# Performance work log

Hardware: AMD Instinct MI355X
Metric: run time of the kernel (lower is better)

The kernel has to match this reference:

```python
import jax, jax.numpy as jnp
import numpy as np

N_NODES = 10000
N_EDGES = 160000
B = 128
HEADS = 4
DIMS = [36, 128, 256, 512]
NEG_SLOPE = 0.2  # PyG GATConv default


def setup_inputs() -> dict:
    key = jax.random.key(0)
    ks = jax.random.split(key, 32)
    inp = {}
    inp["x"] = jax.random.normal(ks[0], (N_NODES, DIMS[0]), jnp.float32)
    inp["edge_index"] = jax.random.randint(ks[1], (2, N_EDGES), 0, N_NODES)
    inp["batch"] = jnp.sort(jax.random.randint(ks[2], (N_NODES,), 0, B))
    ki = 3
    for i in range(3):
        din, dout = DIMS[i], DIMS[i + 1]
        C = dout // HEADS
        inp[f"gcn_w{i}"] = jax.random.normal(ks[ki], (din, dout), jnp.float32) * (din ** -0.5); ki += 1
        inp[f"gcn_b{i}"] = jnp.zeros((dout,), jnp.float32)
        inp[f"gat_w{i}"] = jax.random.normal(ks[ki], (dout, dout), jnp.float32) * (dout ** -0.5); ki += 1
        inp[f"gat_as{i}"] = jax.random.normal(ks[ki], (HEADS, C), jnp.float32) * 0.1; ki += 1
        inp[f"gat_ad{i}"] = jax.random.normal(ks[ki], (HEADS, C), jnp.float32) * 0.1; ki += 1
        inp[f"gat_b{i}"] = jnp.zeros((dout,), jnp.float32)
    D = DIMS[-1]
    inp["ap_w1"] = jax.random.normal(ks[ki], (D, D // 2), jnp.float32) * (D ** -0.5); ki += 1
    inp["ap_b1"] = jnp.zeros((D // 2,), jnp.float32)
    inp["ap_w2"] = jax.random.normal(ks[ki], (D // 2, 1), jnp.float32) * ((D // 2) ** -0.5); ki += 1
    inp["ap_b2"] = jnp.zeros((1,), jnp.float32)
    return inp


def _gcn(x, w, b, src, dst, n):
    # PyG GCNConv: add self-loops, symmetric deg^-1/2 normalization, bias after agg
    h = x @ w  # [N, dout]
    deg = jax.ops.segment_sum(jnp.ones_like(dst, dtype=h.dtype), dst, n) + 1.0  # incl. self-loop
    dinv = deg ** -0.5
    norm = dinv[src] * dinv[dst]  # [E]
    agg = jax.ops.segment_sum(h[src] * norm[:, None], dst, n)
    agg = agg + h * (dinv * dinv)[:, None]  # self-loop messages
    return agg + b


def _gat(x, w, a_s, a_d, b, src, dst, n):
    # PyG GATConv: self-loops, leaky-relu logits, segment softmax over dst, concat heads
    C = w.shape[1] // HEADS
    h = (x @ w).reshape(n, HEADS, C)
    alpha_src = (h * a_s).sum(-1)  # [N, H]
    alpha_dst = (h * a_d).sum(-1)  # [N, H]
    loop = jnp.arange(n)
    s = jnp.concatenate([src, loop])
    d = jnp.concatenate([dst, loop])
    e = jax.nn.leaky_relu(alpha_src[s] + alpha_dst[d], NEG_SLOPE)  # [E+N, H]
    m = jax.ops.segment_max(e, d, n)
    ex = jnp.exp(e - m[d])
    den = jax.ops.segment_sum(ex, d, n)
    alpha = ex / den[d]  # [E+N, H]
    out = jax.ops.segment_sum(h[s] * alpha[:, :, None], d, n)  # [N, H, C]
    return out.reshape(n, HEADS * C) + b


def _forward(x, edge_index, batch, params, ap_w1, ap_b1, ap_w2, ap_b2):
    src, dst = edge_index[0], edge_index[1]
    n = x.shape[0]
    x_in = x
    n_layers = len(params)
    for i, (gw, gb, aw, a_s, a_d, ab) in enumerate(params):
        h = jax.nn.relu(_gcn(x, gw, gb, src, dst, n))  # dropout is identity in eval
        x = h + _gat(h, aw, a_s, a_d, ab, src, dst, n)
        if i < n_layers - 1:
            if x.shape[-1] == x_in.shape[-1]:
                x = x + x_in
            x_in = x
    # attention pooling (global softmax then per-graph masked renorm)
    a = jnp.tanh(x @ ap_w1 + ap_b1) @ ap_w2 + ap_b2  # [N, 1]
    a = jax.nn.softmax(a, axis=0)
    mask = jax.nn.one_hot(batch, B, dtype=x.dtype)  # [N, B]
    aw_ = a * mask
    aw_ = aw_ / (aw_.sum(0, keepdims=True) + 1e-8)
    graph_emb = aw_.T @ x  # [B, D]
    cnt = jax.ops.segment_sum(jnp.ones((n,), x.dtype), batch, B)
    ssum = jax.ops.segment_sum(x, batch, B)
    mean = ssum / jnp.maximum(cnt, 1.0)[:, None]
    smax = jax.ops.segment_max(x, batch, B)
    return jnp.concatenate([graph_emb, mean, smax, ssum], axis=1)  # [B, 4*D]


def reference(x, edge_index, batch,
              gcn_w0, gcn_b0, gat_w0, gat_as0, gat_ad0, gat_b0,
              gcn_w1, gcn_b1, gat_w1, gat_as1, gat_ad1, gat_b1,
              gcn_w2, gcn_b2, gat_w2, gat_as2, gat_ad2, gat_b2,
              ap_w1, ap_b1, ap_w2, ap_b2):
    params = [
        (gcn_w0, gcn_b0, gat_w0, gat_as0, gat_ad0, gat_b0),
        (gcn_w1, gcn_b1, gat_w1, gat_as1, gat_ad1, gat_b1),
        (gcn_w2, gcn_b2, gat_w2, gat_as2, gat_ad2, gat_b2),
    ]
    return _forward(x, edge_index, batch, params, ap_w1, ap_b1, ap_w2, ap_b2)
```

## Files before the change

### kernel.cpp

```cpp
#include <hip/hip_runtime.h>
#include <math.h>

#define NN 10000
#define NE 160000
#define NB 128
#define NH 4
#define DOUT 512
#define NEG 0.2f

typedef __attribute__((ext_vector_type(8))) short short8;
typedef __attribute__((ext_vector_type(4))) float f32x4;
typedef __attribute__((ext_vector_type(4))) unsigned short us4;

__device__ __forceinline__ float leakyf(float v){ return v > 0.f ? v : NEG*v; }
__device__ __forceinline__ void fma4(float4& a, const float4 v, float w){
  a.x += v.x*w; a.y += v.y*w; a.z += v.z*w; a.w += v.w*w;
}
__device__ __forceinline__ unsigned short f2bf(float f){
  unsigned int u = __float_as_uint(f);
  u += 0x7FFFu + ((u >> 16) & 1u);
  return (unsigned short)(u >> 16);
}
__device__ __forceinline__ float bf2f(unsigned short h){
  return __uint_as_float(((unsigned int)h) << 16);
}
__device__ __forceinline__ void split2(float v, unsigned short& h, unsigned short& l){
  h = f2bf(v);
  l = f2bf(v - bf2f(h));
}
__device__ __forceinline__ void store_hl(unsigned short* H, unsigned short* L,
                                         size_t base, float4 v){
  us4 h, l; unsigned short hh, ll;
  split2(v.x, hh, ll); h[0]=hh; l[0]=ll;
  split2(v.y, hh, ll); h[1]=hh; l[1]=ll;
  split2(v.z, hh, ll); h[2]=hh; l[2]=ll;
  split2(v.w, hh, ll); h[3]=hh; l[3]=ll;
  *(us4*)&H[base] = h;
  *(us4*)&L[base] = l;
}
__device__ __forceinline__ float4 load_hl(const unsigned short* __restrict__ H,
                                          const unsigned short* __restrict__ L, size_t base){
  us4 h = *(const us4*)&H[base];
  us4 l = *(const us4*)&L[base];
  return make_float4(bf2f(h[0])+bf2f(l[0]), bf2f(h[1])+bf2f(l[1]),
                     bf2f(h[2])+bf2f(l[2]), bf2f(h[3])+bf2f(l[3]));
}
__device__ __forceinline__ void gl_lds16(const unsigned short* g, unsigned short* l){
  __builtin_amdgcn_global_load_lds(
      (const __attribute__((address_space(1))) unsigned int*)g,
      (__attribute__((address_space(3))) unsigned int*)l, 16, 0, 0);
}

__global__ void k_count(const int* __restrict__ dst, int* __restrict__ cnt){
  int e = blockIdx.x*blockDim.x + threadIdx.x;
  if (e < NE) atomicAdd(&cnt[dst[e]], 1);
}
__global__ void k_scan(const int* __restrict__ cnt, int* __restrict__ rowptr,
                       float* __restrict__ dinv, int* __restrict__ cursor,
                       const int* __restrict__ batch, int* __restrict__ starts){
  __shared__ int part[256];
  const int CH = (NN + 255) / 256;
  int t = threadIdx.x;
  int base = t * CH;
  int s = 0;
  for (int i = 0; i < CH; i++){ int idx = base + i; if (idx < NN) s += cnt[idx]; }
  part[t] = s; __syncthreads();
  for (int o = 1; o < 256; o <<= 1){
    int v = 0;
    if (t >= o) v = part[t - o];
    __syncthreads();
    if (t >= o) part[t] += v;
    __syncthreads();
  }
  int pre = (t == 0) ? 0 : part[t - 1];
  for (int i = 0; i < CH; i++){
    int idx = base + i;
    if (idx < NN){
      int c = cnt[idx];
      rowptr[idx] = pre; pre += c;
      dinv[idx] = rsqrtf((float)c + 1.f);
      cursor[idx] = 0;
    }
  }
  if (t == 255) rowptr[NN] = part[255];
  if (t <= NB){
    int lo = 0, hi = NN;
    while (lo < hi){ int mid = (lo + hi) >> 1; if (batch[mid] < t) lo = mid + 1; else hi = mid; }
    starts[t] = lo;
  }
}
__global__ void k_fill(const int* __restrict__ src, const int* __restrict__ dst,
                       const int* __restrict__ rowptr, int* __restrict__ cursor,
                       int* __restrict__ colidx){
  int e = blockIdx.x*blockDim.x + threadIdx.x;
  if (e >= NE) return;
  int d = dst[e];
  int pos = atomicAdd(&cursor[d], 1);
  colidx[rowptr[d] + pos] = src[e];
}

struct AllConv {
  const float* src[8];
  unsigned short* dh[8];
  unsigned short* dl[8];
  int K[8], Mm[8], Kp[8], tot[8];
};
__global__ void k_convall(AllConv a){
  int j = blockIdx.y;
  int idx = blockIdx.x*blockDim.x + threadIdx.x;
  if (idx >= a.tot[j]) return;
  float v;
  if (j == 0){
    int n = idx >> 6, c = idx & 63;
    v = (c < 36) ? a.src[0][n*36 + c] : 0.f;
  } else {
    int Kp = a.Kp[j], K = a.K[j], M = a.Mm[j];
    int kk = idx % Kp, m = idx / Kp;
    v = (kk < K) ? a.src[j][(size_t)kk*M + m] : 0.f;
  }
  unsigned short h, l; split2(v, h, l);
  a.dh[j][idx] = h; a.dl[j][idx] = l;
}

#define GBM 64
#define GBN 128
#define GBK 32
__global__ __launch_bounds__(256) void k_gemm_bf3(
    const unsigned short* __restrict__ Ah, const unsigned short* __restrict__ Al,
    const unsigned short* __restrict__ Bh, const unsigned short* __restrict__ Bl,
    float* __restrict__ C, int N, int Kp, int M, int mode,
    const float* __restrict__ bias, unsigned short* __restrict__ outH,
    unsigned short* __restrict__ outL,
    const float* __restrict__ a_s, const float* __restrict__ a_d,
    float* __restrict__ as_o, float* __restrict__ ad_o, int Cdim){
  __shared__ unsigned short AsH[GBM*GBK], AsL[GBM*GBK];
  __shared__ unsigned short BsH[GBN*GBK], BsL[GBN*GBK];
  __shared__ float sred[2][GBM][4];
  int gx = M / GBN;
  int gy = (N + GBM - 1) / GBM;
  const int G = 8;
  int bid = blockIdx.x;
  int full = gy / G;
  int bid_full = full * G * gx;
  int by, bx;
  if (bid < bid_full){
    int g = bid / (G*gx); int rem = bid % (G*gx);
    by = g*G + rem % G; bx = rem / G;
  } else {
    int rem = bid - bid_full; int rows = gy - full*G;
    by = full*G + rem % rows; bx = rem / rows;
  }
  int row0 = by * GBM, col0 = bx * GBN;
  int t = threadIdx.x;
  int w = t >> 6, L = t & 63;
  int lm = L & 15, lq = L >> 4;
  int wc = w * 32;

  int sr = L >> 2, sc = L & 3;
  int art = w*16 + sr;
  int ga  = (sc - ((art >> 1) & 3)) & 3;
  int agrow = min(row0 + art, N-1);
  int brt0 = w*16 + sr;
  int brt1 = (w+4)*16 + sr;
  int gb0 = (sc - ((brt0 >> 1) & 3)) & 3;
  int gb1 = (sc - ((brt1 >> 1) & 3)) & 3;
  int bgrow0 = col0 + brt0, bgrow1 = col0 + brt1;

  int rc = (lq + (lm >> 1)) & 3;
  int aoff[4], boff[2];
#pragma unroll
  for (int mi = 0; mi < 4; mi++) aoff[mi] = (mi*16 + lm)*32 + rc*8;
#pragma unroll
  for (int ni = 0; ni < 2; ni++) boff[ni] = (wc + ni*16 + lm)*32 + rc*8;

  f32x4 acc[4][2];
#pragma unroll
  for (int i = 0; i < 4; i++)
#pragma unroll
    for (int j = 0; j < 2; j++) acc[i][j] = (f32x4){0.f,0.f,0.f,0.f};

  int nk = Kp / GBK;
  for (int kt = 0; kt < nk; kt++){
    int k0 = kt * GBK;
    if (kt) __syncthreads();
    gl_lds16(&Ah[(size_t)agrow*Kp + k0 + ga*8],  &AsH[w*512]);
    gl_lds16(&Al[(size_t)agrow*Kp + k0 + ga*8],  &AsL[w*512]);
    gl_lds16(&Bh[(size_t)bgrow0*Kp + k0 + gb0*8], &BsH[w*512]);
    gl_lds16(&Bh[(size_t)bgrow1*Kp + k0 + gb1*8], &BsH[(w+4)*512]);
    gl_lds16(&Bl[(size_t)bgrow0*Kp + k0 + gb0*8], &BsL[w*512]);
    gl_lds16(&Bl[(size_t)bgrow1*Kp + k0 + gb1*8], &BsL[(w+4)*512]);
    __syncthreads();

    short8 ah[4], al[4], bh[2], bl[2];
#pragma unroll
    for (int mi = 0; mi < 4; mi++){
      ah[mi] = *(const short8*)&AsH[aoff[mi]];
      al[mi] = *(const short8*)&AsL[aoff[mi]];
    }
#pragma unroll
    for (int ni = 0; ni < 2; ni++){
      bh[ni] = *(const short8*)&BsH[boff[ni]];
      bl[ni] = *(const short8*)&BsL[boff[ni]];
    }
#pragma unroll
    for (int mi = 0; mi < 4; mi++)
#pragma unroll
      for (int ni = 0; ni < 2; ni++){
        acc[mi][ni] = __builtin_amdgcn_mfma_f32_16x16x32_bf16(ah[mi], bh[ni], acc[mi][ni], 0, 0, 0);
        acc[mi][ni] = __builtin_amdgcn_mfma_f32_16x16x32_bf16(ah[mi], bl[ni], acc[mi][ni], 0, 0, 0);
        acc[mi][ni] = __builtin_amdgcn_mfma_f32_16x16x32_bf16(al[mi], bh[ni], acc[mi][ni], 0, 0, 0);
      }
  }
  if (mode == 1){
#pragma unroll
    for (int mi = 0; mi < 4; mi++)
#pragma unroll
      for (int ni = 0; ni < 2; ni++){
#pragma unroll
        for (int r = 0; r < 4; r++){
          int row = row0 + mi*16 + lq*4 + r;
          int col = col0 + wc + ni*16 + lm;
          if (row < N){
            float v = fmaxf(acc[mi][ni][r] + bias[col], 0.f);
            unsigned short hh, ll; split2(v, hh, ll);
            outH[(size_t)row*M + col] = hh;
            outL[(size_t)row*M + col] = ll;
          }
        }
      }
  } else {
#pragma unroll
    for (int mi = 0; mi < 4; mi++)
#pragma unroll
      for (int ni = 0; ni < 2; ni++){
#pragma unroll
        for (int r = 0; r < 4; r++){
          int row = row0 + mi*16 + lq*4 + r;
          int col = col0 + wc + ni*16 + lm;
          if (row < N) C[(size_t)row*M + col] = acc[mi][ni][r];
        }
      }
  }
  if (mode == 2){
    float sA0 = a_s[col0 + wc + lm], sA1 = a_s[col0 + wc + 16 + lm];
    float dA0 = a_d[col0 + wc + lm], dA1 = a_d[col0 + wc + 16 + lm];
#pragma unroll
    for (int mi = 0; mi < 4; mi++)
#pragma unroll
      for (int r = 0; r < 4; r++){
        float vs = acc[mi][0][r]*sA0 + acc[mi][1][r]*sA1;
        float vd = acc[mi][0][r]*dA0 + acc[mi][1][r]*dA1;
#pragma unroll
        for (int o = 1; o <= 8; o <<= 1){
          vs += __shfl_xor(vs, o);
          vd += __shfl_xor(vd, o);
        }
        if (lm == 0){
          int row = mi*16 + lq*4 + r;
          sred[0][row][w] = vs;
          sred[1][row][w] = vd;
        }
      }
    __syncthreads();
    if (t < GBM){
      int n = row0 + t;
      if (n < N){
        int wph = Cdim >> 5;
        int nheads = 4 / wph;
        for (int g = 0; g < nheads; g++){
          float ss = 0.f, dd = 0.f;
          for (int q = 0; q < wph; q++){
            ss += sred[0][t][g*wph + q];
            dd += sred[1][t][g*wph + q];
          }
          int hd = (col0 + g*wph*32) / Cdim;
          as_o[n*NH + hd] = ss;
          ad_o[n*NH + hd] = dd;
        }
      }
    }
  }
}

__global__ __launch_bounds__(256) void k_gcn_pre(
    const unsigned short* __restrict__ inH, const unsigned short* __restrict__ inL,
    const float* __restrict__ dinv,
    const int* __restrict__ rowptr, const int* __restrict__ colidx,
    unsigned short* __restrict__ outH, unsigned short* __restrict__ outL,
    int Kp, int nchunk){
  int bid = blockIdx.x;
  int chunk = bid % nchunk, grp = bid / nchunk;
  int t = threadIdx.x;
  int sub = t & 15;
  int n = grp*16 + (t >> 4);
  if (n >= NN) return;
  int f0 = chunk*64 + sub*4;
  int b = rowptr[n], e = rowptr[n+1];
  float dn = dinv[n];
  float4 a0 = make_float4(0,0,0,0), a1 = make_float4(0,0,0,0);
  float4 a2 = make_float4(0,0,0,0), a3 = make_float4(0,0,0,0);
  int j = b;
  for (; j + 3 < e; j += 4){
    int s0 = colidx[j], s1 = colidx[j+1], s2 = colidx[j+2], s3 = colidx[j+3];
    float w0 = dinv[s0], w1 = dinv[s1], w2 = dinv[s2], w3 = dinv[s3];
    float4 v0 = load_hl(inH, inL, (size_t)s0*Kp + f0);
    float4 v1 = load_hl(inH, inL, (size_t)s1*Kp + f0);
    float4 v2 = load_hl(inH, inL, (size_t)s2*Kp + f0);
    float4 v3 = load_hl(inH, inL, (size_t)s3*Kp + f0);
    fma4(a0, v0, w0*dn); fma4(a1, v1, w1*dn);
    fma4(a2, v2, w2*dn); fma4(a3, v3, w3*dn);
  }
  for (; j < e; j++){
    int s = colidx[j];
    float4 v = load_hl(inH, inL, (size_t)s*Kp + f0);
    fma4(a0, v, dinv[s]*dn);
  }
  float4 acc = make_float4(a0.x+a1.x+a2.x+a3.x, a0.y+a1.y+a2.y+a3.y,
                           a0.z+a1.z+a2.z+a3.z, a0.w+a1.w+a2.w+a3.w);
  float4 sv = load_hl(inH, inL, (size_t)n*Kp + f0);
  float dn2 = dn*dn;
  acc.x += sv.x*dn2; acc.y += sv.y*dn2; acc.z += sv.z*dn2; acc.w += sv.w*dn2;
  store_hl(outH, outL, (size_t)n*Kp + f0, acc);
}

__global__ void k_gat_maxden(const int* __restrict__ rowptr, const int* __restrict__ colidx,
                             const float* __restrict__ as_, const float* __restrict__ ad_,
                             float* __restrict__ eself, float* __restrict__ den,
                             float* __restrict__ ealpha){
  int idx = blockIdx.x*blockDim.x + threadIdx.x;
  if (idx >= NN*NH) return;
  int n = idx >> 2, hd = idx & 3;
  float adn = ad_[idx];
  float selflog = leakyf(as_[idx] + adn);
  int b = rowptr[n], e = rowptr[n+1];
  float m0 = selflog, m1 = -INFINITY, m2 = -INFINITY, m3 = -INFINITY;
  int j = b;
  for (; j + 3 < e; j += 4){
    int s0 = colidx[j], s1 = colidx[j+1], s2 = colidx[j+2], s3 = colidx[j+3];
    float l0 = leakyf(as_[s0*NH + hd] + adn), l1 = leakyf(as_[s1*NH + hd] + adn);
    float l2 = leakyf(as_[s2*NH + hd] + adn), l3 = leakyf(as_[s3*NH + hd] + adn);
    ealpha[(size_t)(j+0)*NH + hd] = l0; ealpha[(size_t)(j+1)*NH + hd] = l1;
    ealpha[(size_t)(j+2)*NH + hd] = l2; ealpha[(size_t)(j+3)*NH + hd] = l3;
    m0 = fmaxf(m0, l0); m1 = fmaxf(m1, l1);
    m2 = fmaxf(m2, l2); m3 = fmaxf(m3, l3);
  }
  for (; j < e; j++){
    float l = leakyf(as_[colidx[j]*NH + hd] + adn);
    ealpha[(size_t)j*NH + hd] = l;
    m0 = fmaxf(m0, l);
  }
  float m = fmaxf(fmaxf(m0, m1), fmaxf(m2, m3));
  float es = expf(selflog - m);
  float d0 = es, d1 = 0.f, d2 = 0.f, d3 = 0.f;
  j = b;
  for (; j + 3 < e; j += 4){
    float v0 = expf(ealpha[(size_t)(j+0)*NH + hd] - m);
    float v1 = expf(ealpha[(size_t)(j+1)*NH + hd] - m);
    float v2 = expf(ealpha[(size_t)(j+2)*NH + hd] - m);
    float v3 = expf(ealpha[(size_t)(j+3)*NH + hd] - m);
    ealpha[(size_t)(j+0)*NH + hd] = v0; ealpha[(size_t)(j+1)*NH + hd] = v1;
    ealpha[(size_t)(j+2)*NH + hd] = v2; ealpha[(size_t)(j+3)*NH + hd] = v3;
    d0 += v0; d1 += v1; d2 += v2; d3 += v3;
  }
  for (; j < e; j++){
    float v = expf(ealpha[(size_t)j*NH + hd] - m);
    ealpha[(size_t)j*NH + hd] = v;
    d0 += v;
  }
  eself[idx] = es;
  den[idx] = (d0 + d1) + (d2 + d3);
}
__global__ __launch_bounds__(256) void k_gat_gather(
    const float* __restrict__ hg,
    const unsigned short* __restrict__ inH, const unsigned short* __restrict__ inL,
    const int* __restrict__ rowptr, const int* __restrict__ colidx,
    const float* __restrict__ ealpha, const float* __restrict__ eself,
    const float* __restrict__ den, const float* __restrict__ ab,
    unsigned short* __restrict__ outH, unsigned short* __restrict__ outL,
    int M, int C, int nchunk){
  int bid = blockIdx.x;
  int chunk = bid % nchunk, grp = bid / nchunk;
  int t = threadIdx.x;
  int sub = t & 15;
  int n = grp*16 + (t >> 4);
  if (n >= NN) return;
  int f0 = chunk*64 + sub*4;
  int hd = f0 / C;
  int b = rowptr[n], e = rowptr[n+1];
  float4 a0 = make_float4(0,0,0,0), a1 = make_float4(0,0,0,0);
  float4 a2 = make_float4(0,0,0,0), a3 = make_float4(0,0,0,0);
  int j = b;
  for (; j + 3 < e; j += 4){
    int s0 = colidx[j], s1 = colidx[j+1], s2 = colidx[j+2], s3 = colidx[j+3];
    float e0 = ealpha[(size_t)(j+0)*NH + hd], e1 = ealpha[(size_t)(j+1)*NH + hd];
    float e2 = ealpha[(size_t)(j+2)*NH + hd], e3 = ealpha[(size_t)(j+3)*NH + hd];
    float4 v0 = *(const float4*)&hg[(size_t)s0*M + f0];
    float4 v1 = *(const float4*)&hg[(size_t)s1*M + f0];
    float4 v2 = *(const float4*)&hg[(size_t)s2*M + f0];
    float4 v3 = *(const float4*)&hg[(size_t)s3*M + f0];
    fma4(a0, v0, e0); fma4(a1, v1, e1);
    fma4(a2, v2, e2); fma4(a3, v3, e3);
  }
  for (; j < e; j++){
    int s = colidx[j];
    float4 v = *(const float4*)&hg[(size_t)s*M + f0];
    fma4(a0, v, ealpha[(size_t)j*NH + hd]);
  }
  float4 acc = make_float4(a0.x+a1.x+a2.x+a3.x, a0.y+a1.y+a2.y+a3.y,
                           a0.z+a1.z+a2.z+a3.z, a0.w+a1.w+a2.w+a3.w);
  int ai = n*NH + hd;
  float es = eself[ai], inv = 1.f/den[ai];
  float4 sv = *(const float4*)&hg[(size_t)n*M + f0];
  float4 hv = load_hl(inH, inL, (size_t)n*M + f0);
  float4 bb = *(const float4*)&ab[f0];
  float4 r = make_float4(
    hv.x + bb.x + (sv.x*es + acc.x)*inv,
    hv.y + bb.y + (sv.y*es + acc.y)*inv,
    hv.z + bb.z + (sv.z*es + acc.z)*inv,
    hv.w + bb.w + (sv.w*es + acc.w)*inv);
  store_hl(outH, outL, (size_t)n*M + f0, r);
}

__global__ void k_tanh_dot(const float* __restrict__ t1, const float* __restrict__ b1,
                           const float* __restrict__ w2, const float* __restrict__ b2,
                           float* __restrict__ apre){
  int n = blockIdx.x, t = threadIdx.x;
  float4 v  = ((const float4*)(t1 + (size_t)n*256))[t];
  float4 bb = ((const float4*)b1)[t];
  float4 ww = ((const float4*)w2)[t];
  float s = tanhf(v.x+bb.x)*ww.x + tanhf(v.y+bb.y)*ww.y
          + tanhf(v.z+bb.z)*ww.z + tanhf(v.w+bb.w)*ww.w;
  for (int o = 32; o > 0; o >>= 1) s += __shfl_xor(s, o);
  if (t == 0) apre[n] = s + b2[0];
}
__global__ void k_pool_prep(const float* __restrict__ apre, const int* __restrict__ starts,
                            float* __restrict__ pw){
  int g = blockIdx.x, t = threadIdx.x;
  int b = starts[g], e = starts[g+1];
  float m = -INFINITY;
  for (int n = b + t; n < e; n += 64) m = fmaxf(m, apre[n]);
  for (int o = 32; o > 0; o >>= 1) m = fmaxf(m, __shfl_xor(m, o));
  float s = 0.f;
  for (int n = b + t; n < e; n += 64) s += expf(apre[n] - m);
  for (int o = 32; o > 0; o >>= 1) s += __shfl_xor(s, o);
  float inv = 1.f / (s + 1e-8f);
  for (int n = b + t; n < e; n += 64) pw[n] = expf(apre[n] - m) * inv;
}
__global__ void k_pool(const unsigned short* __restrict__ xH, const unsigned short* __restrict__ xL,
                       const float* __restrict__ pw, const int* __restrict__ starts,
                       float* __restrict__ out){
  int g = blockIdx.x, t = threadIdx.x;
  int b = starts[g], e = starts[g+1];
  float4 sum = make_float4(0,0,0,0), wacc = make_float4(0,0,0,0);
  float4 mx = make_float4(-INFINITY,-INFINITY,-INFINITY,-INFINITY);
  for (int n = b; n < e; n++){
    float4 xv = load_hl(xH, xL, (size_t)n*DOUT + t*4);
    float p = pw[n];
    sum.x += xv.x; sum.y += xv.y; sum.z += xv.z; sum.w += xv.w;
    mx.x = fmaxf(mx.x, xv.x); mx.y = fmaxf(mx.y, xv.y);
    mx.z = fmaxf(mx.z, xv.z); mx.w = fmaxf(mx.w, xv.w);
    fma4(wacc, xv, p);
  }
  float ic = 1.f / fmaxf((float)(e - b), 1.f);
  float4* o = (float4*)(out + (size_t)g*4*DOUT);
  o[t]       = wacc;
  o[128 + t] = make_float4(sum.x*ic, sum.y*ic, sum.z*ic, sum.w*ic);
  o[256 + t] = mx;
  o[384 + t] = sum;
}

extern "C" void kernel_launch(void* const* d_in, const int* in_sizes, int n_in,
                              void* d_out, int out_size, void* d_ws, size_t ws_size,
                              hipStream_t stream) {
  const float* x0   = (const float*)d_in[0];
  const int*   ei   = (const int*)d_in[1];
  const int*   src  = ei;
  const int*   dst  = ei + NE;
  const int*   batch= (const int*)d_in[2];
  const float* gw[3]  = {(const float*)d_in[3],  (const float*)d_in[9],  (const float*)d_in[15]};
  const float* gb[3]  = {(const float*)d_in[4],  (const float*)d_in[10], (const float*)d_in[16]};
  const float* aw[3]  = {(const float*)d_in[5],  (const float*)d_in[11], (const float*)d_in[17]};
  const float* asw[3] = {(const float*)d_in[6],  (const float*)d_in[12], (const float*)d_in[18]};
  const float* adw[3] = {(const float*)d_in[7],  (const float*)d_in[13], (const float*)d_in[19]};
  const float* ab[3]  = {(const float*)d_in[8],  (const float*)d_in[14], (const float*)d_in[20]};
  const float* apw1 = (const float*)d_in[21];
  const float* apb1 = (const float*)d_in[22];
  const float* apw2 = (const float*)d_in[23];
  const float* apb2 = (const float*)d_in[24];
  float* out = (float*)d_out;

  char* p = (char*)d_ws;
  auto alloc = [&](size_t bytes) -> void* {
    void* r = (void*)p; p += (bytes + 255) & ~(size_t)255; return r;
  };
  float* f1 = (float*)alloc((size_t)NN*512*4);
  unsigned short* actH0 = (unsigned short*)alloc((size_t)NN*512*2);
  unsigned short* actL0 = (unsigned short*)alloc((size_t)NN*512*2);
  unsigned short* actH1 = (unsigned short*)alloc((size_t)NN*512*2);
  unsigned short* actL1 = (unsigned short*)alloc((size_t)NN*512*2);
  unsigned short* preH  = (unsigned short*)alloc((size_t)NN*256*2);
  unsigned short* preL  = (unsigned short*)alloc((size_t)NN*256*2);
  unsigned short* x0h = (unsigned short*)alloc((size_t)NN*64*2);
  unsigned short* x0l = (unsigned short*)alloc((size_t)NN*64*2);
  const int wK[7]  = {36, 128, 128, 256, 256, 512, 512};
  const int wM[7]  = {128, 128, 256, 256, 512, 512, 256};
  const int wKp[7] = {64, 128, 128, 256, 256, 512, 512};
  const float* wsrc[7] = {gw[0], aw[0], gw[1], aw[1], gw[2], aw[2], apw1};
  unsigned short* wTh[7]; unsigned short* wTl[7];
  for (int i = 0; i < 7; i++){
    size_t sz = (size_t)wM[i]*wKp[i]*2;
    wTh[i] = (unsigned short*)alloc(sz);
    wTl[i] = (unsigned short*)alloc(sz);
  }
  float* ealpha = (float*)alloc((size_t)NE*NH*4);
  float* dinv = (float*)alloc(NN*4);
  float* as_  = (float*)alloc(NN*NH*4);
  float* ad_  = (float*)alloc(NN*NH*4);
  float* eself= (float*)alloc(NN*NH*4);
  float* den  = (float*)alloc(NN*NH*4);
  float* apre = (float*)alloc(NN*4);
  float* pw   = (float*)alloc(NN*4);
  int* rowptr = (int*)alloc((NN+1)*4);
  int* colidx = (int*)alloc((size_t)NE*4);
  int* cnt    = (int*)alloc(NN*4);
  int* cursor = (int*)alloc(NN*4);
  int* starts = (int*)alloc((NB+1)*4);

  hipMemsetAsync(cnt, 0, NN*sizeof(int), stream);
  k_count<<<(NE+255)/256, 256, 0, stream>>>(dst, cnt);
  k_scan<<<1, 256, 0, stream>>>(cnt, rowptr, dinv, cursor, batch, starts);
  k_fill<<<(NE+255)/256, 256, 0, stream>>>(src, dst, rowptr, cursor, colidx);

  AllConv ac;
  ac.src[0] = x0; ac.dh[0] = x0h; ac.dl[0] = x0l;
  ac.K[0] = 36; ac.Mm[0] = NN; ac.Kp[0] = 64; ac.tot[0] = NN*64;
  int maxtot = NN*64;
  for (int i = 0; i < 7; i++){
    ac.src[i+1] = wsrc[i]; ac.dh[i+1] = wTh[i]; ac.dl[i+1] = wTl[i];
    ac.K[i+1] = wK[i]; ac.Mm[i+1] = wM[i]; ac.Kp[i+1] = wKp[i];
    ac.tot[i+1] = wKp[i]*wM[i];
    if (ac.tot[i+1] > maxtot) maxtot = ac.tot[i+1];
  }
  k_convall<<<dim3((maxtot+255)/256, 8), 256, 0, stream>>>(ac);

  const int dims[4] = {36, 128, 256, 512};
  const int ngrp = (NN + 15) / 16;
  const unsigned short* curH = x0h; const unsigned short* curL = x0l;
  int wi = 0;
  for (int i = 0; i < 3; i++){
    int Kin = (i == 0) ? 64 : dims[i];
    int M = dims[i+1], C = M/NH;
    int nchunk_in = Kin / 64;
    int nchunk = M / 64;
    int nblk = (M/GBN) * ((NN+GBM-1)/GBM);
    k_gcn_pre<<<nchunk_in*ngrp, 256, 0, stream>>>(curH, curL, dinv, rowptr, colidx,
                                                  preH, preL, Kin, nchunk_in);
    k_gemm_bf3<<<nblk, 256, 0, stream>>>(preH, preL, wTh[wi], wTl[wi], f1, NN, wKp[wi], M,
                                         1, gb[i], actH0, actL0,
                                         nullptr, nullptr, nullptr, nullptr, C);
    wi++;
    k_gemm_bf3<<<nblk, 256, 0, stream>>>(actH0, actL0, wTh[wi], wTl[wi], f1, NN, wKp[wi], M,
                                         2, nullptr, nullptr, nullptr,
                                         asw[i], adw[i], as_, ad_, C);
    wi++;
    k_gat_maxden<<<(NN*NH+255)/256, 256, 0, stream>>>(rowptr, colidx, as_, ad_, eself, den, ealpha);
    k_gat_gather<<<nchunk*ngrp, 256, 0, stream>>>(f1, actH0, actL0, rowptr, colidx,
                                                  ealpha, eself, den, ab[i],
                                                  actH1, actL1, M, C, nchunk);
    curH = actH1; curL = actL1;
  }

  {
    int nblk = (256/GBN) * ((NN+GBM-1)/GBM);
    k_gemm_bf3<<<nblk, 256, 0, stream>>>(actH1, actL1, wTh[6], wTl[6], f1, NN, wKp[6], 256,
                                         0, nullptr, nullptr, nullptr,
                                         nullptr, nullptr, nullptr, nullptr, 64);
  }
  k_tanh_dot<<<NN, 64, 0, stream>>>(f1, apb1, apw2, apb2, apre);
  k_pool_prep<<<NB, 64, 0, stream>>>(apre, starts, pw);
  k_pool<<<NB, 128, 0, stream>>>(actH1, actL1, pw, starts, out);
}
```

Baseline: 465.1 us.

## Fuse attention-pool tanh into GEMM epilogue and use online softmax for GAT

Adds a GEMM epilogue mode that applies tanh, dots with the second pooling weight and atomically accumulates per-node scores. This removes the f1 store and the separate tanh kernel. GAT max/denominator becomes a single-pass online softmax that stores raw logits and the max, and the gather kernel recomputes exp. The pool prep kernel is merged into the pool kernel, and the scalar output bias is dropped since softmax is shift-invariant. The exp recomputation in the gather adds redundant transcendental work per feature chunk.

Result: faster. 455.9 us (-2.0%).

```diff
diff --git a/kernel.cpp b/kernel.cpp
--- a/kernel.cpp
+++ b/kernel.cpp
@@ -228,7 +228,7 @@
           }
         }
       }
-  } else {
+  } else if (mode != 3){
 #pragma unroll
     for (int mi = 0; mi < 4; mi++)
 #pragma unroll
@@ -277,6 +277,26 @@
           as_o[n*NH + hd] = ss;
           ad_o[n*NH + hd] = dd;
         }
+      }
+    }
+  } else if (mode == 3){
+    float b0 = bias[col0 + wc + lm], b1v = bias[col0 + wc + 16 + lm];
+    float w0v = a_s[col0 + wc + lm], w1v = a_s[col0 + wc + 16 + lm];
+#pragma unroll
+    for (int mi = 0; mi < 4; mi++)
+#pragma unroll
+      for (int r = 0; r < 4; r++){
+        float v = tanhf(acc[mi][0][r] + b0)*w0v + tanhf(acc[mi][1][r] + b1v)*w1v;
+#pragma unroll
+        for (int o = 1; o <= 8; o <<= 1) v += __shfl_xor(v, o);
+        if (lm == 0) sred[0][mi*16 + lq*4 + r][w] = v;
+      }
+    __syncthreads();
+    if (t < GBM){
+      int n = row0 + t;
+      if (n < N){
+        float s = sred[0][t][0] + sred[0][t][1] + sred[0][t][2] + sred[0][t][3];
+        atomicAdd(&as_o[n], s);
       }
     }
   }
@@ -326,14 +346,14 @@
 __global__ void k_gat_maxden(const int* __restrict__ rowptr, const int* __restrict__ colidx,
                              const float* __restrict__ as_, const float* __restrict__ ad_,
                              float* __restrict__ eself, float* __restrict__ den,
-                             float* __restrict__ ealpha){
+                             float* __restrict__ mmax, float* __restrict__ ealpha){
   int idx = blockIdx.x*blockDim.x + threadIdx.x;
   if (idx >= NN*NH) return;
   int n = idx >> 2, hd = idx & 3;
   float adn = ad_[idx];
   float selflog = leakyf(as_[idx] + adn);
   int b = rowptr[n], e = rowptr[n+1];
-  float m0 = selflog, m1 = -INFINITY, m2 = -INFINITY, m3 = -INFINITY;
+  float m = selflog, d = 1.f;
   int j = b;
   for (; j + 3 < e; j += 4){
     int s0 = colidx[j], s1 = colidx[j+1], s2 = colidx[j+2], s3 = colidx[j+3];
@@ -341,41 +361,27 @@
     float l2 = leakyf(as_[s2*NH + hd] + adn), l3 = leakyf(as_[s3*NH + hd] + adn);
     ealpha[(size_t)(j+0)*NH + hd] = l0; ealpha[(size_t)(j+1)*NH + hd] = l1;
     ealpha[(size_t)(j+2)*NH + hd] = l2; ealpha[(size_t)(j+3)*NH + hd] = l3;
-    m0 = fmaxf(m0, l0); m1 = fmaxf(m1, l1);
-    m2 = fmaxf(m2, l2); m3 = fmaxf(m3, l3);
+    float m4 = fmaxf(fmaxf(l0, l1), fmaxf(l2, l3));
+    if (m4 > m){ d *= expf(m - m4); m = m4; }
+    d += expf(l0 - m) + expf(l1 - m) + expf(l2 - m) + expf(l3 - m);
   }
   for (; j < e; j++){
     float l = leakyf(as_[colidx[j]*NH + hd] + adn);
     ealpha[(size_t)j*NH + hd] = l;
-    m0 = fmaxf(m0, l);
-  }
-  float m = fmaxf(fmaxf(m0, m1), fmaxf(m2, m3));
-  float es = expf(selflog - m);
-  float d0 = es, d1 = 0.f, d2 = 0.f, d3 = 0.f;
-  j = b;
-  for (; j + 3 < e; j += 4){
-    float v0 = expf(ealpha[(size_t)(j+0)*NH + hd] - m);
-    float v1 = expf(ealpha[(size_t)(j+1)*NH + hd] - m);
-    float v2 = expf(ealpha[(size_t)(j+2)*NH + hd] - m);
-    float v3 = expf(ealpha[(size_t)(j+3)*NH + hd] - m);
-    ealpha[(size_t)(j+0)*NH + hd] = v0; ealpha[(size_t)(j+1)*NH + hd] = v1;
-    ealpha[(size_t)(j+2)*NH + hd] = v2; ealpha[(size_t)(j+3)*NH + hd] = v3;
-    d0 += v0; d1 += v1; d2 += v2; d3 += v3;
-  }
-  for (; j < e; j++){
-    float v = expf(ealpha[(size_t)j*NH + hd] - m);
-    ealpha[(size_t)j*NH + hd] = v;
-    d0 += v;
-  }
-  eself[idx] = es;
-  den[idx] = (d0 + d1) + (d2 + d3);
+    if (l > m){ d *= expf(m - l); m = l; }
+    d += expf(l - m);
+  }
+  eself[idx] = expf(selflog - m);
+  den[idx] = d;
+  mmax[idx] = m;
 }
 __global__ __launch_bounds__(256) void k_gat_gather(
     const float* __restrict__ hg,
     const unsigned short* __restrict__ inH, const unsigned short* __restrict__ inL,
     const int* __restrict__ rowptr, const int* __restrict__ colidx,
     const float* __restrict__ ealpha, const float* __restrict__ eself,
-    const float* __restrict__ den, const float* __restrict__ ab,
+    const float* __restrict__ den, const float* __restrict__ mmax,
+    const float* __restrict__ ab,
     unsigned short* __restrict__ outH, unsigned short* __restrict__ outL,
     int M, int C, int nchunk){
   int bid = blockIdx.x;
@@ -387,13 +393,17 @@
   int f0 = chunk*64 + sub*4;
   int hd = f0 / C;
   int b = rowptr[n], e = rowptr[n+1];
+  int ai = n*NH + hd;
+  float mm = mmax[ai];
   float4 a0 = make_float4(0,0,0,0), a1 = make_float4(0,0,0,0);
   float4 a2 = make_float4(0,0,0,0), a3 = make_float4(0,0,0,0);
   int j = b;
   for (; j + 3 < e; j += 4){
     int s0 = colidx[j], s1 = colidx[j+1], s2 = colidx[j+2], s3 = colidx[j+3];
-    float e0 = ealpha[(size_t)(j+0)*NH + hd], e1 = ealpha[(size_t)(j+1)*NH + hd];
-    float e2 = ealpha[(size_t)(j+2)*NH + hd], e3 = ealpha[(size_t)(j+3)*NH + hd];
+    float e0 = expf(ealpha[(size_t)(j+0)*NH + hd] - mm);
+    float e1 = expf(ealpha[(size_t)(j+1)*NH + hd] - mm);
+    float e2 = expf(ealpha[(size_t)(j+2)*NH + hd] - mm);
+    float e3 = expf(ealpha[(size_t)(j+3)*NH + hd] - mm);
     float4 v0 = *(const float4*)&hg[(size_t)s0*M + f0];
     float4 v1 = *(const float4*)&hg[(size_t)s1*M + f0];
     float4 v2 = *(const float4*)&hg[(size_t)s2*M + f0];
@@ -404,11 +414,10 @@
   for (; j < e; j++){
     int s = colidx[j];
     float4 v = *(const float4*)&hg[(size_t)s*M + f0];
-    fma4(a0, v, ealpha[(size_t)j*NH + hd]);
+    fma4(a0, v, expf(ealpha[(size_t)j*NH + hd] - mm));
   }
   float4 acc = make_float4(a0.x+a1.x+a2.x+a3.x, a0.y+a1.y+a2.y+a3.y,
                            a0.z+a1.z+a2.z+a3.z, a0.w+a1.w+a2.w+a3.w);
-  int ai = n*NH + hd;
   float es = eself[ai], inv = 1.f/den[ai];
   float4 sv = *(const float4*)&hg[(size_t)n*M + f0];
   float4 hv = load_hl(inH, inL, (size_t)n*M + f0);
@@ -421,41 +430,33 @@
   store_hl(outH, outL, (size_t)n*M + f0, r);
 }
 
-__global__ void k_tanh_dot(const float* __restrict__ t1, const float* __restrict__ b1,
-                           const float* __restrict__ w2, const float* __restrict__ b2,
-                           float* __restrict__ apre){
-  int n = blockIdx.x, t = threadIdx.x;
-  float4 v  = ((const float4*)(t1 + (size_t)n*256))[t];
-  float4 bb = ((const float4*)b1)[t];
-  float4 ww = ((const float4*)w2)[t];
-  float s = tanhf(v.x+bb.x)*ww.x + tanhf(v.y+bb.y)*ww.y
-          + tanhf(v.z+bb.z)*ww.z + tanhf(v.w+bb.w)*ww.w;
-  for (int o = 32; o > 0; o >>= 1) s += __shfl_xor(s, o);
-  if (t == 0) apre[n] = s + b2[0];
-}
-__global__ void k_pool_prep(const float* __restrict__ apre, const int* __restrict__ starts,
-                            float* __restrict__ pw){
+__global__ void k_pool(const unsigned short* __restrict__ xH, const unsigned short* __restrict__ xL,
+                       const float* __restrict__ apre, const int* __restrict__ starts,
+                       float* __restrict__ out){
+  __shared__ float red[128];
   int g = blockIdx.x, t = threadIdx.x;
   int b = starts[g], e = starts[g+1];
   float m = -INFINITY;
-  for (int n = b + t; n < e; n += 64) m = fmaxf(m, apre[n]);
-  for (int o = 32; o > 0; o >>= 1) m = fmaxf(m, __shfl_xor(m, o));
+  for (int n = b + t; n < e; n += 128) m = fmaxf(m, apre[n]);
+  red[t] = m; __syncthreads();
+  for (int o = 64; o > 0; o >>= 1){
+    if (t < o) red[t] = fmaxf(red[t], red[t + o]);
+    __syncthreads();
+  }
+  m = red[0]; __syncthreads();
   float s = 0.f;
-  for (int n = b + t; n < e; n += 64) s += expf(apre[n] - m);
-  for (int o = 32; o > 0; o >>= 1) s += __shfl_xor(s, o);
-  float inv = 1.f / (s + 1e-8f);
-  for (int n = b + t; n < e; n += 64) pw[n] = expf(apre[n] - m) * inv;
-}
-__global__ void k_pool(const unsigned short* __restrict__ xH, const unsigned short* __restrict__ xL,
-                       const float* __restrict__ pw, const int* __restrict__ starts,
-                       float* __restrict__ out){
-  int g = blockIdx.x, t = threadIdx.x;
-  int b = starts[g], e = starts[g+1];
+  for (int n = b + t; n < e; n += 128) s += expf(apre[n] - m);
+  red[t] = s; __syncthreads();
+  for (int o = 64; o > 0; o >>= 1){
+    if (t < o) red[t] += red[t + o];
+    __syncthreads();
+  }
+  float inv = 1.f / (red[0] + 1e-8f);
   float4 sum = make_float4(0,0,0,0), wacc = make_float4(0,0,0,0);
   float4 mx = make_float4(-INFINITY,-INFINITY,-INFINITY,-INFINITY);
   for (int n = b; n < e; n++){
     float4 xv = load_hl(xH, xL, (size_t)n*DOUT + t*4);
-    float p = pw[n];
+    float p = expf(apre[n] - m) * inv;
     sum.x += xv.x; sum.y += xv.y; sum.z += xv.z; sum.w += xv.w;
     mx.x = fmaxf(mx.x, xv.x); mx.y = fmaxf(mx.y, xv.y);
     mx.z = fmaxf(mx.z, xv.z); mx.w = fmaxf(mx.w, xv.w);
@@ -486,7 +487,6 @@
   const float* apw1 = (const float*)d_in[21];
   const float* apb1 = (const float*)d_in[22];
   const float* apw2 = (const float*)d_in[23];
-  const float* apb2 = (const float*)d_in[24];
   float* out = (float*)d_out;
 
   char* p = (char*)d_ws;
@@ -518,8 +518,8 @@
   float* ad_  = (float*)alloc(NN*NH*4);
   float* eself= (float*)alloc(NN*NH*4);
   float* den  = (float*)alloc(NN*NH*4);
+  float* mmax = (float*)alloc(NN*NH*4);
   float* apre = (float*)alloc(NN*4);
-  float* pw   = (float*)alloc(NN*4);
   int* rowptr = (int*)alloc((NN+1)*4);
   int* colidx = (int*)alloc((size_t)NE*4);
   int* cnt    = (int*)alloc(NN*4);
@@ -563,20 +563,20 @@
                                          2, nullptr, nullptr, nullptr,
                                          asw[i], adw[i], as_, ad_, C);
     wi++;
-    k_gat_maxden<<<(NN*NH+255)/256, 256, 0, stream>>>(rowptr, colidx, as_, ad_, eself, den, ealpha);
+    k_gat_maxden<<<(NN*NH+255)/256, 256, 0, stream>>>(rowptr, colidx, as_, ad_,
+                                                      eself, den, mmax, ealpha);
     k_gat_gather<<<nchunk*ngrp, 256, 0, stream>>>(f1, actH0, actL0, rowptr, colidx,
-                                                  ealpha, eself, den, ab[i],
+                                                  ealpha, eself, den, mmax, ab[i],
                                                   actH1, actL1, M, C, nchunk);
     curH = actH1; curL = actL1;
   }
 
+  hipMemsetAsync(apre, 0, NN*sizeof(float), stream);
   {
     int nblk = (256/GBN) * ((NN+GBM-1)/GBM);
     k_gemm_bf3<<<nblk, 256, 0, stream>>>(actH1, actL1, wTh[6], wTl[6], f1, NN, wKp[6], 256,
-                                         0, nullptr, nullptr, nullptr,
-                                         nullptr, nullptr, nullptr, nullptr, 64);
-  }
-  k_tanh_dot<<<NN, 64, 0, stream>>>(f1, apb1, apw2, apb2, apre);
-  k_pool_prep<<<NB, 64, 0, stream>>>(apre, starts, pw);
-  k_pool<<<NB, 128, 0, stream>>>(actH1, actL1, pw, starts, out);
-}
+                                         3, apb1, nullptr, nullptr,
+                                         apw2, nullptr, apre, nullptr, 64);
+  }
+  k_pool<<<NB, 128, 0, stream>>>(actH1, actL1, apre, starts, out);
+}
```
